# Kernel optimization log

Hardware: AMD Instinct MI355X
Metric: run time of the kernel (lower is better)

The kernel has to match this reference:

```python
import jax, jax.numpy as jnp
import numpy as np

N_NODES = 50000
N_EDGES = 500000
D_IN = 128
HID = 128
OUT = 2
N_REL = 4
BN_EPS = 1e-5


def setup_inputs() -> dict:
    key = jax.random.key(0)
    ks = jax.random.split(key, 14)
    s_in = 1.0 / np.sqrt(D_IN)
    s_h = 1.0 / np.sqrt(HID)
    return {
        "x": jax.random.normal(ks[0], (N_NODES, D_IN), jnp.float32),
        "edge_index": jax.random.randint(ks[1], (N_REL, 2, N_EDGES), 0, N_NODES, jnp.int32),
        "W1": jax.random.normal(ks[2], (N_REL, D_IN, HID), jnp.float32) * s_in,
        "b1": jax.random.normal(ks[3], (N_REL, HID), jnp.float32) * s_in,
        "W2": jax.random.normal(ks[4], (N_REL, HID, HID), jnp.float32) * s_h,
        "b2": jax.random.normal(ks[5], (N_REL, HID), jnp.float32) * s_h,
        "bn_gamma": jnp.ones((HID,), jnp.float32),
        "bn_beta": jnp.zeros((HID,), jnp.float32),
        "lin1_W": jax.random.normal(ks[6], (HID, HID), jnp.float32) * s_h,
        "lin1_b": jax.random.normal(ks[7], (HID,), jnp.float32) * s_h,
        "lin2_W": jax.random.normal(ks[8], (HID, OUT), jnp.float32) * s_h,
        "lin2_b": jax.random.normal(ks[9], (OUT,), jnp.float32) * s_h,
    }


def _gcn(x, ei, W, b):
    # GCNConv: D^-1/2 (A + I) D^-1/2 (X W) + b
    n = x.shape[0]
    h = x @ W                                    # [N, H]
    loops = jnp.arange(n, dtype=ei.dtype)
    src = jnp.concatenate([ei[0], loops])        # add self loops
    dst = jnp.concatenate([ei[1], loops])
    deg = jax.ops.segment_sum(jnp.ones(dst.shape, h.dtype), dst, num_segments=n)
    dinv = jnp.where(deg > 0, jax.lax.rsqrt(deg), 0.0)
    norm = dinv[src] * dinv[dst]                 # [E+N]
    msg = h[src] * norm[:, None]                 # gather + scale
    return jax.ops.segment_sum(msg, dst, num_segments=n) + b


def _hetero(x, edge_index, W, b):
    # HeteroConv with aggr='sum' over the 4 relation types (same src/dst node type)
    out = _gcn(x, edge_index[0], W[0], b[0])
    for r in range(1, N_REL):
        out = out + _gcn(x, edge_index[r], W[r], b[r])
    return out


def reference(x, edge_index, W1, b1, W2, b2, bn_gamma, bn_beta, lin1_W, lin1_b, lin2_W, lin2_b):
    h = jax.nn.relu(_hetero(x, edge_index, W1, b1))
    h = jax.nn.relu(_hetero(h, edge_index, W2, b2))
    # BatchNorm1d (batch statistics, biased variance)
    mean = h.mean(axis=0)
    var = h.var(axis=0)
    h = (h - mean) * jax.lax.rsqrt(var + BN_EPS) * bn_gamma + bn_beta
    h = jax.nn.relu(h @ lin1_W + lin1_b)
    # dropout is identity in eval
    return h @ lin2_W + lin2_b
```

## Files before the change

### kernel.cpp

```cpp
#include <hip/hip_runtime.h>
#include <math.h>

#define NN 50000
#define NE 500000
#define NREL 4
#define D 128
#define RSZ 512
#define NRANGE 98
#define NBK (NREL * NRANGE)
#define BCAP 6144
#define NCH 128
#define CH 3907
#define FCAP 96
#define CAST_BLKS 6250
static constexpr float BN_EPS = 1e-5f;

typedef __attribute__((ext_vector_type(8))) _Float16 half8;
typedef __attribute__((ext_vector_type(4))) float f32x4;

__device__ __forceinline__ unsigned short f2h_bits(float f) {
    _Float16 h = (_Float16)f;
    return __builtin_bit_cast(unsigned short, h);
}
__device__ __forceinline__ float hi2f(unsigned p) {
    return (float)__builtin_bit_cast(_Float16, (unsigned short)(p >> 16));
}

__global__ __launch_bounds__(256) void k_pre(const float* __restrict__ x,
                                             const float* __restrict__ W1, const float* __restrict__ W2,
                                             const float* __restrict__ l1W, const float* __restrict__ b1,
                                             const float* __restrict__ b2,
                                             unsigned short* __restrict__ xb,
                                             unsigned short* __restrict__ Wt1,
                                             unsigned short* __restrict__ Wt2,
                                             unsigned short* __restrict__ Wt3,
                                             float* __restrict__ bs1, float* __restrict__ bs2,
                                             float* __restrict__ bnsum) {
    int blk = blockIdx.x, tid = threadIdx.x;
    if (blk < CAST_BLKS) {
        int i = blk * 256 + tid;
        float4 v = *(const float4*)(x + (size_t)i * 4);
        unsigned short u[4] = {f2h_bits(v.x), f2h_bits(v.y), f2h_bits(v.z), f2h_bits(v.w)};
        *(ushort4*)(xb + (size_t)i * 4) = *(ushort4*)u;
    } else if (blk < CAST_BLKS + 256) {
        int i = (blk - CAST_BLKS) * 256 + tid;
        int kk = i & 511, n = i >> 9;
        Wt1[n * 512 + kk] = f2h_bits(W1[kk * 128 + n]);
        Wt2[n * 512 + kk] = f2h_bits(W2[kk * 128 + n]);
    } else if (blk < CAST_BLKS + 320) {
        int i = (blk - CAST_BLKS - 256) * 256 + tid;
        int kk = i & 127, n = i >> 7;
        Wt3[n * 128 + kk] = f2h_bits(l1W[kk * 128 + n]);
    } else {
        if (tid < 128) {
            bs1[tid] = b1[tid] + b1[128 + tid] + b1[256 + tid] + b1[384 + tid];
            bs2[tid] = b2[tid] + b2[128 + tid] + b2[256 + tid] + b2[384 + tid];
        }
        bnsum[tid] = 0.f;
    }
}

__global__ __launch_bounds__(256) void k_bin(const int* __restrict__ ei,
                                             int* __restrict__ frag,
                                             int* __restrict__ cntg) {
    int c = blockIdx.x, r = blockIdx.y;
    const int* srcp = ei + r * 2 * NE;
    const int* dstp = srcp + NE;
    __shared__ int bins[NRANGE * FCAP];
    __shared__ int cnt[NRANGE];
    int tid = threadIdx.x;
    for (int i = tid; i < NRANGE; i += 256) cnt[i] = 0;
    __syncthreads();
    int e0 = c * CH, e1 = min(e0 + CH, NE);
    for (int e = e0 + tid; e < e1; e += 256) {
        int d = dstp[e];
        int s = srcp[e];
        int q = d >> 9;
        int pos = atomicAdd(&cnt[q], 1);
        if (pos < FCAP) bins[q * FCAP + pos] = s | ((d & 511) << 16);
    }
    __syncthreads();
    int w = tid >> 6, lane = tid & 63;
    for (int q = w; q < NRANGE; q += 4) {
        int k = min(cnt[q], FCAP);
        int gbase = ((r * NRANGE + q) * NCH + c) * FCAP;
        for (int i = lane; i < k; i += 64) frag[gbase + i] = bins[q * FCAP + i];
    }
    for (int q = tid; q < NRANGE; q += 256) cntg[(r * NRANGE + q) * NCH + c] = min(cnt[q], FCAP);
}

__global__ __launch_bounds__(512) void k_sortb(const int* __restrict__ frag,
                                               const int* __restrict__ cntg,
                                               unsigned short* __restrict__ csr,
                                               int* __restrict__ rstart,
                                               int* __restrict__ rend,
                                               float* __restrict__ dinv) {
    int q = blockIdx.x, r = blockIdx.y;
    int blk = r * NRANGE + q;
    int n0 = q * RSZ;
    int nrows = min(RSZ, NN - n0);
    __shared__ int cnts[NCH], cbase[NCH];
    __shared__ int stage[BCAP];
    __shared__ unsigned short csr_s[BCAP];
    __shared__ int hist[RSZ], off[RSZ], cnt2[RSZ];
    int tid = threadIdx.x;
    hist[tid] = 0;
    cnt2[tid] = 0;
    if (tid < NCH) cnts[tid] = cntg[blk * NCH + tid];
    __syncthreads();
    if (tid < NCH) cbase[tid] = cnts[tid];
    __syncthreads();
    for (int d = 1; d < NCH; d <<= 1) {
        int t = 0;
        if (tid < NCH && tid >= d) t = cbase[tid - d];
        __syncthreads();
        if (tid < NCH) cbase[tid] += t;
        __syncthreads();
    }
    if (tid < NCH) cbase[tid] -= cnts[tid];
    __syncthreads();
    int tot = cbase[NCH - 1] + cnts[NCH - 1];
    {
        int g = tid >> 2, l = tid & 3;
        int k = cnts[g], cb = cbase[g];
        int gbase = (blk * NCH + g) * FCAP;
        for (int i = l; i < k; i += 4)
            if (cb + i < BCAP) stage[cb + i] = frag[gbase + i];
    }
    __syncthreads();
    if (tot > BCAP) tot = BCAP;
    for (int i = tid; i < tot; i += 512) atomicAdd(&hist[(stage[i] >> 16) & 511], 1);
    __syncthreads();
    int h = hist[tid];
    if (tid < nrows) dinv[r * NN + n0 + tid] = rsqrtf((float)(h + 1));
    off[tid] = h;
    __syncthreads();
    for (int d = 1; d < RSZ; d <<= 1) {
        int t = (tid >= d) ? off[tid - d] : 0;
        __syncthreads();
        off[tid] += t;
        __syncthreads();
    }
    int excl = off[tid] - h;
    __syncthreads();
    off[tid] = excl;
    int base = blk * BCAP;
    if (tid < nrows) {
        rstart[r * NN + n0 + tid] = base + excl;
        rend[r * NN + n0 + tid] = base + excl + h;
    }
    __syncthreads();
    for (int i = tid; i < tot; i += 512) {
        int v = stage[i];
        int dl = (v >> 16) & 511;
        int p = atomicAdd(&cnt2[dl], 1);
        csr_s[off[dl] + p] = (unsigned short)(v & 0xFFFF);
    }
    __syncthreads();
    for (int i = tid; i < tot; i += 512) csr[base + i] = csr_s[i];
}

__global__ __launch_bounds__(256) void k_wei(const unsigned short* __restrict__ csr,
                                             const float* __restrict__ dinv,
                                             unsigned* __restrict__ wpack) {
    int gi = blockIdx.x * 256 + threadIdx.x;
    int r = gi / (NRANGE * BCAP);
    int s = csr[gi];
    float w = dinv[r * NN + min(s, NN - 1)];
    wpack[gi] = (unsigned)s | ((unsigned)f2h_bits(w) << 16);
}

__global__ __launch_bounds__(256) void k_agg(const unsigned short* __restrict__ in,
                                             const unsigned* __restrict__ wpack,
                                             const int* __restrict__ rstart,
                                             const int* __restrict__ rend,
                                             const float* __restrict__ dinv,
                                             unsigned short* __restrict__ Acat) {
    int wave = threadIdx.x >> 6, lane = threadIdx.x & 63;
    int n = blockIdx.x * 4 + wave;
    if (n >= NN) return;
    int t = lane & 15;
    int base = lane & 48;
    int nb = (base >> 4) * NN + n;
    const half8* in8 = (const half8*)in;
    float wn = dinv[nb];
    int start = rstart[nb];
    int deg = rend[nb] - start;
    int dm = deg;
    dm = max(dm, __shfl_xor(dm, 16));
    dm = max(dm, __shfl_xor(dm, 32));
    half8 us = in8[(size_t)n * 16 + t];
    float a[8];
#pragma unroll
    for (int j = 0; j < 8; j++) a[j] = wn * (float)us[j];

    for (int w0 = 0; w0 < dm; w0 += 16) {
        int li = w0 + t;
        int gi = min(start + li, NBK * BCAP - 1);
        unsigned pv = wpack[gi];
        if (li >= deg) pv = 0u;
        unsigned p0 = __shfl(pv, base + 0), p1 = __shfl(pv, base + 1);
        unsigned p2 = __shfl(pv, base + 2), p3 = __shfl(pv, base + 3);
        unsigned p4 = __shfl(pv, base + 4), p5 = __shfl(pv, base + 5);
        unsigned p6 = __shfl(pv, base + 6), p7 = __shfl(pv, base + 7);
        {
            half8 r0 = in8[(p0 & 0xFFFFu) * 16 + t];
            half8 r1 = in8[(p1 & 0xFFFFu) * 16 + t];
            half8 r2 = in8[(p2 & 0xFFFFu) * 16 + t];
            half8 r3 = in8[(p3 & 0xFFFFu) * 16 + t];
            half8 r4 = in8[(p4 & 0xFFFFu) * 16 + t];
            half8 r5 = in8[(p5 & 0xFFFFu) * 16 + t];
            half8 r6 = in8[(p6 & 0xFFFFu) * 16 + t];
            half8 r7 = in8[(p7 & 0xFFFFu) * 16 + t];
            float w0f = hi2f(p0), w1f = hi2f(p1), w2f = hi2f(p2), w3f = hi2f(p3);
            float w4f = hi2f(p4), w5f = hi2f(p5), w6f = hi2f(p6), w7f = hi2f(p7);
#pragma unroll
            for (int j = 0; j < 8; j++) a[j] = fmaf((float)r0[j], w0f, a[j]);
#pragma unroll
            for (int j = 0; j < 8; j++) a[j] = fmaf((float)r1[j], w1f, a[j]);
#pragma unroll
            for (int j = 0; j < 8; j++) a[j] = fmaf((float)r2[j], w2f, a[j]);
#pragma unroll
            for (int j = 0; j < 8; j++) a[j] = fmaf((float)r3[j], w3f, a[j]);
#pragma unroll
            for (int j = 0; j < 8; j++) a[j] = fmaf((float)r4[j], w4f, a[j]);
#pragma unroll
            for (int j = 0; j < 8; j++) a[j] = fmaf((float)r5[j], w5f, a[j]);
#pragma unroll
            for (int j = 0; j < 8; j++) a[j] = fmaf((float)r6[j], w6f, a[j]);
#pragma unroll
            for (int j = 0; j < 8; j++) a[j] = fmaf((float)r7[j], w7f, a[j]);
        }
        if (w0 + 8 >= dm) continue;
        p0 = __shfl(pv, base + 8);  p1 = __shfl(pv, base + 9);
        p2 = __shfl(pv, base + 10); p3 = __shfl(pv, base + 11);
        p4 = __shfl(pv, base + 12); p5 = __shfl(pv, base + 13);
        p6 = __shfl(pv, base + 14); p7 = __shfl(pv, base + 15);
        {
            half8 r0 = in8[(p0 & 0xFFFFu) * 16 + t];
            half8 r1 = in8[(p1 & 0xFFFFu) * 16 + t];
            half8 r2 = in8[(p2 & 0xFFFFu) * 16 + t];
            half8 r3 = in8[(p3 & 0xFFFFu) * 16 + t];
            half8 r4 = in8[(p4 & 0xFFFFu) * 16 + t];
            half8 r5 = in8[(p5 & 0xFFFFu) * 16 + t];
            half8 r6 = in8[(p6 & 0xFFFFu) * 16 + t];
            half8 r7 = in8[(p7 & 0xFFFFu) * 16 + t];
            float w0f = hi2f(p0), w1f = hi2f(p1), w2f = hi2f(p2), w3f = hi2f(p3);
            float w4f = hi2f(p4), w5f = hi2f(p5), w6f = hi2f(p6), w7f = hi2f(p7);
#pragma unroll
            for (int j = 0; j < 8; j++) a[j] = fmaf((float)r0[j], w0f, a[j]);
#pragma unroll
            for (int j = 0; j < 8; j++) a[j] = fmaf((float)r1[j], w1f, a[j]);
#pragma unroll
            for (int j = 0; j < 8; j++) a[j] = fmaf((float)r2[j], w2f, a[j]);
#pragma unroll
            for (int j = 0; j < 8; j++) a[j] = fmaf((float)r3[j], w3f, a[j]);
#pragma unroll
            for (int j = 0; j < 8; j++) a[j] = fmaf((float)r4[j], w4f, a[j]);
#pragma unroll
            for (int j = 0; j < 8; j++) a[j] = fmaf((float)r5[j], w5f, a[j]);
#pragma unroll
            for (int j = 0; j < 8; j++) a[j] = fmaf((float)r6[j], w6f, a[j]);
#pragma unroll
            for (int j = 0; j < 8; j++) a[j] = fmaf((float)r7[j], w7f, a[j]);
        }
    }
    _Float16 ob[8];
#pragma unroll
    for (int j = 0; j < 8; j++) ob[j] = (_Float16)(wn * a[j]);
    *(half8*)(Acat + (size_t)n * 512 + (base << 3) + t * 8) = *(half8*)ob;
}

template <int K, bool STATS>
__global__ __launch_bounds__(256) void k_mm(const unsigned short* __restrict__ A,
                                            const unsigned short* __restrict__ Bt,
                                            const float* __restrict__ bias,
                                            unsigned short* __restrict__ C,
                                            float* __restrict__ bnsum) {
    int tid = threadIdx.x;
    int w = tid >> 6, lane = tid & 63;
    int ln = lane & 15, quad = lane >> 4;
    int mwave = blockIdx.x * 256 + w * 64;

    f32x4 acc[4][8];
#pragma unroll
    for (int a = 0; a < 4; a++)
#pragma unroll
        for (int b = 0; b < 8; b++) acc[a][b] = (f32x4){0.f, 0.f, 0.f, 0.f};

    size_t arow[4];
#pragma unroll
    for (int mf = 0; mf < 4; mf++) {
        int m = mwave + mf * 16 + ln;
        arow[mf] = (size_t)min(m, NN - 1) * K;
    }
    size_t brow[8];
#pragma unroll
    for (int nf = 0; nf < 8; nf++) brow[nf] = (size_t)(nf * 16 + ln) * K;

    for (int k0 = 0; k0 < K; k0 += 32) {
        int kof = k0 + quad * 8;
        half8 af[4], bf[8];
#pragma unroll
        for (int mf = 0; mf < 4; mf++) af[mf] = *(const half8*)(A + arow[mf] + kof);
#pragma unroll
        for (int nf = 0; nf < 8; nf++) bf[nf] = *(const half8*)(Bt + brow[nf] + kof);
#pragma unroll
        for (int mf = 0; mf < 4; mf++)
#pragma unroll
            for (int nf = 0; nf < 8; nf++)
                acc[mf][nf] = __builtin_amdgcn_mfma_f32_16x16x32_f16(af[mf], bf[nf], acc[mf][nf], 0, 0, 0);
    }

    float bs[8];
#pragma unroll
    for (int nf = 0; nf < 8; nf++) bs[nf] = bias[nf * 16 + ln];
    float sn[8], qn[8];
#pragma unroll
    for (int nf = 0; nf < 8; nf++) { sn[nf] = 0.f; qn[nf] = 0.f; }

#pragma unroll
    for (int mf = 0; mf < 4; mf++)
#pragma unroll
        for (int nf = 0; nf < 8; nf++)
#pragma unroll
            for (int rg = 0; rg < 4; rg++) {
                int m = mwave + mf * 16 + quad * 4 + rg;
                if (m < NN) {
                    float v = fmaxf(acc[mf][nf][rg] + bs[nf], 0.f);
                    if (STATS) { sn[nf] += v; qn[nf] += v * v; }
                    C[(size_t)m * 128 + nf * 16 + ln] = f2h_bits(v);
                }
            }

    if (STATS) {
#pragma unroll
        for (int nf = 0; nf < 8; nf++) {
            float s = sn[nf], q = qn[nf];
            s += __shfl_xor(s, 16); s += __shfl_xor(s, 32);
            q += __shfl_xor(q, 16); q += __shfl_xor(q, 32);
            if (quad == 0) {
                unsafeAtomicAdd(&bnsum[nf * 16 + ln], s);
                unsafeAtomicAdd(&bnsum[128 + nf * 16 + ln], q);
            }
        }
    }
}

__global__ __launch_bounds__(256) void k_final(const unsigned short* __restrict__ R2,
                                               const float* __restrict__ bnsum,
                                               const float* __restrict__ gamma,
                                               const float* __restrict__ beta,
                                               const unsigned short* __restrict__ Wt3,
                                               const float* __restrict__ l1b,
                                               const float* __restrict__ l2W,
                                               const float* __restrict__ l2b,
                                               float* __restrict__ out) {
    __shared__ float bnp_s[256];
    int tid = threadIdx.x;
    if (tid < 128) {
        float mean = bnsum[tid] / (float)NN;
        float var = bnsum[128 + tid] / (float)NN - mean * mean;
        float sc = gamma[tid] * rsqrtf(var + BN_EPS);
        bnp_s[tid] = sc;
        bnp_s[128 + tid] = beta[tid] - mean * sc;
    }
    __syncthreads();
    int w = tid >> 6, lane = tid & 63;
    int ln = lane & 15, quad = lane >> 4;
    int mwave = blockIdx.x * 256 + w * 64;

    f32x4 acc[4][8];
#pragma unroll
    for (int a = 0; a < 4; a++)
#pragma unroll
        for (int b = 0; b < 8; b++) acc[a][b] = (f32x4){0.f, 0.f, 0.f, 0.f};

    size_t arow[4];
#pragma unroll
    for (int mf = 0; mf < 4; mf++) {
        int m = mwave + mf * 16 + ln;
        arow[mf] = (size_t)min(m, NN - 1) * 128;
    }
    size_t brow[8];
#pragma unroll
    for (int nf = 0; nf < 8; nf++) brow[nf] = (size_t)(nf * 16 + ln) * 128;

    for (int k0 = 0; k0 < 128; k0 += 32) {
        int kof = k0 + quad * 8;
        float scv[8], shv[8];
#pragma unroll
        for (int j = 0; j < 8; j++) {
            scv[j] = bnp_s[kof + j];
            shv[j] = bnp_s[128 + kof + j];
        }
        half8 af[4], bf[8];
#pragma unroll
        for (int mf = 0; mf < 4; mf++) {
            half8 rv = *(const half8*)(R2 + arow[mf] + kof);
            _Float16 ab[8];
#pragma unroll
            for (int j = 0; j < 8; j++)
                ab[j] = (_Float16)(fmaf((float)rv[j], scv[j], shv[j]));
            af[mf] = *(half8*)ab;
        }
#pragma unroll
        for (int nf = 0; nf < 8; nf++) bf[nf] = *(const half8*)(Wt3 + brow[nf] + kof);
#pragma unroll
        for (int mf = 0; mf < 4; mf++)
#pragma unroll
            for (int nf = 0; nf < 8; nf++)
                acc[mf][nf] = __builtin_amdgcn_mfma_f32_16x16x32_f16(af[mf], bf[nf], acc[mf][nf], 0, 0, 0);
    }

    float b1v[8], w0[8], w1[8];
#pragma unroll
    for (int nf = 0; nf < 8; nf++) {
        int n = nf * 16 + ln;
        b1v[nf] = l1b[n];
        w0[nf] = l2W[n * 2];
        w1[nf] = l2W[n * 2 + 1];
    }
    float ob0 = l2b[0], ob1 = l2b[1];
#pragma unroll
    for (int mf = 0; mf < 4; mf++)
#pragma unroll
        for (int rg = 0; rg < 4; rg++) {
            float p0 = 0.f, p1 = 0.f;
#pragma unroll
            for (int nf = 0; nf < 8; nf++) {
                float y = fmaxf(acc[mf][nf][rg] + b1v[nf], 0.f);
                p0 += y * w0[nf];
                p1 += y * w1[nf];
            }
            p0 += __shfl_xor(p0, 1); p0 += __shfl_xor(p0, 2);
            p0 += __shfl_xor(p0, 4); p0 += __shfl_xor(p0, 8);
            p1 += __shfl_xor(p1, 1); p1 += __shfl_xor(p1, 2);
            p1 += __shfl_xor(p1, 4); p1 += __shfl_xor(p1, 8);
            int m = mwave + mf * 16 + quad * 4 + rg;
            if (ln == 0 && m < NN) {
                out[(size_t)m * 2 + 0] = p0 + ob0;
                out[(size_t)m * 2 + 1] = p1 + ob1;
            }
        }
}

extern "C" void kernel_launch(void* const* d_in, const int* in_sizes, int n_in,
                              void* d_out, int out_size, void* d_ws, size_t ws_size,
                              hipStream_t stream) {
    const float* x = (const float*)d_in[0];
    const int* ei = (const int*)d_in[1];
    const float* W1 = (const float*)d_in[2];
    const float* b1 = (const float*)d_in[3];
    const float* W2 = (const float*)d_in[4];
    const float* b2 = (const float*)d_in[5];
    const float* gamma = (const float*)d_in[6];
    const float* beta = (const float*)d_in[7];
    const float* l1W = (const float*)d_in[8];
    const float* l1b = (const float*)d_in[9];
    const float* l2W = (const float*)d_in[10];
    const float* l2b = (const float*)d_in[11];
    float* out = (float*)d_out;

    char* ws = (char*)d_ws;
    size_t off = 0;
    auto alloc = [&](size_t bytes) {
        void* p = ws + off;
        off += (bytes + 255) & ~(size_t)255;
        return p;
    };
    float* dinv = (float*)alloc((size_t)NREL * NN * sizeof(float));
    int* rstart = (int*)alloc((size_t)NREL * NN * sizeof(int));
    int* rend = (int*)alloc((size_t)NREL * NN * sizeof(int));
    unsigned short* csr = (unsigned short*)alloc((size_t)NBK * BCAP * 2);
    unsigned short* xb = (unsigned short*)alloc((size_t)NN * D * 2);
    unsigned short* Acat = (unsigned short*)alloc((size_t)NN * 512 * 2);
    unsigned short* h1b = (unsigned short*)alloc((size_t)NN * D * 2);
    unsigned short* R2b = (unsigned short*)alloc((size_t)NN * D * 2);
    unsigned short* Wt1 = (unsigned short*)alloc(128 * 512 * 2);
    unsigned short* Wt2 = (unsigned short*)alloc(128 * 512 * 2);
    unsigned short* Wt3 = (unsigned short*)alloc(128 * 128 * 2);
    float* bs1 = (float*)alloc(128 * sizeof(float));
    float* bs2 = (float*)alloc(128 * sizeof(float));
    float* bnsum = (float*)alloc(256 * sizeof(float));

    int* frag = (int*)Acat;
    int* cntg = frag + (size_t)NREL * NRANGE * NCH * FCAP;
    unsigned* wpack = (unsigned*)R2b;

    k_pre<<<CAST_BLKS + 321, 256, 0, stream>>>(x, W1, W2, l1W, b1, b2, xb, Wt1, Wt2, Wt3,
                                               bs1, bs2, bnsum);
    dim3 bgrid(NCH, NREL);
    k_bin<<<bgrid, 256, 0, stream>>>(ei, frag, cntg);
    dim3 sgrid(NRANGE, NREL);
    k_sortb<<<sgrid, 512, 0, stream>>>(frag, cntg, csr, rstart, rend, dinv);
    k_wei<<<(NBK * BCAP) / 256, 256, 0, stream>>>(csr, dinv, wpack);

    int agrid = (NN + 3) / 4;
    k_agg<<<agrid, 256, 0, stream>>>(xb, wpack, rstart, rend, dinv, Acat);
    k_mm<512, false><<<(NN + 255) / 256, 256, 0, stream>>>(Acat, Wt1, bs1, h1b, nullptr);
    k_agg<<<agrid, 256, 0, stream>>>(h1b, wpack, rstart, rend, dinv, Acat);
    k_mm<512, true><<<(NN + 255) / 256, 256, 0, stream>>>(Acat, Wt2, bs2, R2b, bnsum);
    k_final<<<(NN + 255) / 256, 256, 0, stream>>>(R2b, bnsum, gamma, beta, Wt3, l1b, l2W, l2b, out);
}
```

Baseline: 367.8 us.

## Fuse neighbor aggregation with MFMA matmul via shared-memory tile

```diff
diff --git a/kernel.cpp b/kernel.cpp
--- a/kernel.cpp
+++ b/kernel.cpp
@@ -13,6 +13,9 @@
 #define CH 3907
 #define FCAP 96
 #define CAST_BLKS 6250
+#define TN 32
+#define NPW 8
+#define NTILE ((NN + TN - 1) / TN)
 static constexpr float BN_EPS = 1e-5f;
 
 typedef __attribute__((ext_vector_type(8))) _Float16 half8;
@@ -170,178 +173,191 @@
     wpack[gi] = (unsigned)s | ((unsigned)f2h_bits(w) << 16);
 }
 
-__global__ __launch_bounds__(256) void k_agg(const unsigned short* __restrict__ in,
-                                             const unsigned* __restrict__ wpack,
-                                             const int* __restrict__ rstart,
-                                             const int* __restrict__ rend,
-                                             const float* __restrict__ dinv,
-                                             unsigned short* __restrict__ Acat) {
-    int wave = threadIdx.x >> 6, lane = threadIdx.x & 63;
-    int n = blockIdx.x * 4 + wave;
-    if (n >= NN) return;
+template <bool STATS>
+__global__ __launch_bounds__(256) void k_fused(const unsigned short* __restrict__ in,
+                                               const unsigned* __restrict__ wpack,
+                                               const int* __restrict__ rstart,
+                                               const int* __restrict__ rend,
+                                               const float* __restrict__ dinv,
+                                               const unsigned short* __restrict__ Bt,
+                                               const float* __restrict__ bias,
+                                               unsigned short* __restrict__ C,
+                                               float* __restrict__ bnsum) {
+    __shared__ unsigned short A_s[TN * 512];
+    int tid = threadIdx.x;
+    int wave = tid >> 6, lane = tid & 63;
     int t = lane & 15;
     int base = lane & 48;
-    int nb = (base >> 4) * NN + n;
+    int q = base >> 4;
+    int tile = blockIdx.x;
     const half8* in8 = (const half8*)in;
-    float wn = dinv[nb];
-    int start = rstart[nb];
-    int deg = rend[nb] - start;
-    int dm = deg;
-    dm = max(dm, __shfl_xor(dm, 16));
-    dm = max(dm, __shfl_xor(dm, 32));
-    half8 us = in8[(size_t)n * 16 + t];
-    float a[8];
-#pragma unroll
-    for (int j = 0; j < 8; j++) a[j] = wn * (float)us[j];
-
-    for (int w0 = 0; w0 < dm; w0 += 16) {
-        int li = w0 + t;
-        int gi = min(start + li, NBK * BCAP - 1);
-        unsigned pv = wpack[gi];
-        if (li >= deg) pv = 0u;
-        unsigned p0 = __shfl(pv, base + 0), p1 = __shfl(pv, base + 1);
-        unsigned p2 = __shfl(pv, base + 2), p3 = __shfl(pv, base + 3);
-        unsigned p4 = __shfl(pv, base + 4), p5 = __shfl(pv, base + 5);
-        unsigned p6 = __shfl(pv, base + 6), p7 = __shfl(pv, base + 7);
-        {
-            half8 r0 = in8[(p0 & 0xFFFFu) * 16 + t];
-            half8 r1 = in8[(p1 & 0xFFFFu) * 16 + t];
-            half8 r2 = in8[(p2 & 0xFFFFu) * 16 + t];
-            half8 r3 = in8[(p3 & 0xFFFFu) * 16 + t];
-            half8 r4 = in8[(p4 & 0xFFFFu) * 16 + t];
-            half8 r5 = in8[(p5 & 0xFFFFu) * 16 + t];
-            half8 r6 = in8[(p6 & 0xFFFFu) * 16 + t];
-            half8 r7 = in8[(p7 & 0xFFFFu) * 16 + t];
-            float w0f = hi2f(p0), w1f = hi2f(p1), w2f = hi2f(p2), w3f = hi2f(p3);
-            float w4f = hi2f(p4), w5f = hi2f(p5), w6f = hi2f(p6), w7f = hi2f(p7);
-#pragma unroll
-            for (int j = 0; j < 8; j++) a[j] = fmaf((float)r0[j], w0f, a[j]);
-#pragma unroll
-            for (int j = 0; j < 8; j++) a[j] = fmaf((float)r1[j], w1f, a[j]);
-#pragma unroll
-            for (int j = 0; j < 8; j++) a[j] = fmaf((float)r2[j], w2f, a[j]);
-#pragma unroll
-            for (int j = 0; j < 8; j++) a[j] = fmaf((float)r3[j], w3f, a[j]);
-#pragma unroll
-            for (int j = 0; j < 8; j++) a[j] = fmaf((float)r4[j], w4f, a[j]);
-#pragma unroll
-            for (int j = 0; j < 8; j++) a[j] = fmaf((float)r5[j], w5f, a[j]);
-#pragma unroll
-            for (int j = 0; j < 8; j++) a[j] = fmaf((float)r6[j], w6f, a[j]);
-#pragma unroll
-            for (int j = 0; j < 8; j++) a[j] = fmaf((float)r7[j], w7f, a[j]);
-        }
-        if (w0 + 8 >= dm) continue;
-        p0 = __shfl(pv, base + 8);  p1 = __shfl(pv, base + 9);
-        p2 = __shfl(pv, base + 10); p3 = __shfl(pv, base + 11);
-        p4 = __shfl(pv, base + 12); p5 = __shfl(pv, base + 13);
-        p6 = __shfl(pv, base + 14); p7 = __shfl(pv, base + 15);
-        {
-            half8 r0 = in8[(p0 & 0xFFFFu) * 16 + t];
-            half8 r1 = in8[(p1 & 0xFFFFu) * 16 + t];
-            half8 r2 = in8[(p2 & 0xFFFFu) * 16 + t];
-            half8 r3 = in8[(p3 & 0xFFFFu) * 16 + t];
-            half8 r4 = in8[(p4 & 0xFFFFu) * 16 + t];
-            half8 r5 = in8[(p5 & 0xFFFFu) * 16 + t];
-            half8 r6 = in8[(p6 & 0xFFFFu) * 16 + t];
-            half8 r7 = in8[(p7 & 0xFFFFu) * 16 + t];
-            float w0f = hi2f(p0), w1f = hi2f(p1), w2f = hi2f(p2), w3f = hi2f(p3);
-            float w4f = hi2f(p4), w5f = hi2f(p5), w6f = hi2f(p6), w7f = hi2f(p7);
-#pragma unroll
-            for (int j = 0; j < 8; j++) a[j] = fmaf((float)r0[j], w0f, a[j]);
-#pragma unroll
-            for (int j = 0; j < 8; j++) a[j] = fmaf((float)r1[j], w1f, a[j]);
-#pragma unroll
-            for (int j = 0; j < 8; j++) a[j] = fmaf((float)r2[j], w2f, a[j]);
-#pragma unroll
-            for (int j = 0; j < 8; j++) a[j] = fmaf((float)r3[j], w3f, a[j]);
-#pragma unroll
-            for (int j = 0; j < 8; j++) a[j] = fmaf((float)r4[j], w4f, a[j]);
-#pragma unroll
-            for (int j = 0; j < 8; j++) a[j] = fmaf((float)r5[j], w5f, a[j]);
-#pragma unroll
-            for (int j = 0; j < 8; j++) a[j] = fmaf((float)r6[j], w6f, a[j]);
-#pragma unroll
-            for (int j = 0; j < 8; j++) a[j] = fmaf((float)r7[j], w7f, a[j]);
-        }
-    }
-    _Float16 ob[8];
-#pragma unroll
-    for (int j = 0; j < 8; j++) ob[j] = (_Float16)(wn * a[j]);
-    *(half8*)(Acat + (size_t)n * 512 + (base << 3) + t * 8) = *(half8*)ob;
-}
-
-template <int K, bool STATS>
-__global__ __launch_bounds__(256) void k_mm(const unsigned short* __restrict__ A,
-                                            const unsigned short* __restrict__ Bt,
-                                            const float* __restrict__ bias,
-                                            unsigned short* __restrict__ C,
-                                            float* __restrict__ bnsum) {
-    int tid = threadIdx.x;
-    int w = tid >> 6, lane = tid & 63;
+    int nbq = q * NN;
+
+    int row0 = wave * NPW;
+    {
+        int n0 = tile * TN + row0;
+        int nc0 = min(n0, NN - 1);
+        int sP = rstart[nbq + nc0];
+        int eP = rend[nbq + nc0];
+        float wP = dinv[nbq + nc0];
+        half8 uP = in8[(size_t)nc0 * 16 + t];
+        for (int i = 0; i < NPW; ++i) {
+            int row = row0 + i;
+            int n = tile * TN + row;
+            bool valid = (n < NN);
+            int start = sP;
+            int deg = valid ? (eP - sP) : 0;
+            float wn = valid ? wP : 0.f;
+            half8 us = uP;
+            if (i + 1 < NPW) {
+                int nn = min(n + 1, NN - 1);
+                sP = rstart[nbq + nn];
+                eP = rend[nbq + nn];
+                wP = dinv[nbq + nn];
+                uP = in8[(size_t)nn * 16 + t];
+            }
+            int dm = deg;
+            dm = max(dm, __shfl_xor(dm, 16));
+            dm = max(dm, __shfl_xor(dm, 32));
+            float a[8];
+#pragma unroll
+            for (int j = 0; j < 8; j++) a[j] = wn * (float)us[j];
+
+            for (int w0 = 0; w0 < dm; w0 += 16) {
+                int li = w0 + t;
+                int gi = min(start + li, NBK * BCAP - 1);
+                unsigned pv = wpack[gi];
+                if (li >= deg) pv = 0u;
+                unsigned p0 = __shfl(pv, base + 0), p1 = __shfl(pv, base + 1);
+                unsigned p2 = __shfl(pv, base + 2), p3 = __shfl(pv, base + 3);
+                unsigned p4 = __shfl(pv, base + 4), p5 = __shfl(pv, base + 5);
+                unsigned p6 = __shfl(pv, base + 6), p7 = __shfl(pv, base + 7);
+                {
+                    half8 r0 = in8[(p0 & 0xFFFFu) * 16 + t];
+                    half8 r1 = in8[(p1 & 0xFFFFu) * 16 + t];
+                    half8 r2 = in8[(p2 & 0xFFFFu) * 16 + t];
+                    half8 r3 = in8[(p3 & 0xFFFFu) * 16 + t];
+                    half8 r4 = in8[(p4 & 0xFFFFu) * 16 + t];
+                    half8 r5 = in8[(p5 & 0xFFFFu) * 16 + t];
+                    half8 r6 = in8[(p6 & 0xFFFFu) * 16 + t];
+                    half8 r7 = in8[(p7 & 0xFFFFu) * 16 + t];
+                    float w0f = hi2f(p0), w1f = hi2f(p1), w2f = hi2f(p2), w3f = hi2f(p3);
+                    float w4f = hi2f(p4), w5f = hi2f(p5), w6f = hi2f(p6), w7f = hi2f(p7);
+#pragma unroll
+                    for (int j = 0; j < 8; j++) a[j] = fmaf((float)r0[j], w0f, a[j]);
+#pragma unroll
+                    for (int j = 0; j < 8; j++) a[j] = fmaf((float)r1[j], w1f, a[j]);
+#pragma unroll
+                    for (int j = 0; j < 8; j++) a[j] = fmaf((float)r2[j], w2f, a[j]);
+#pragma unroll
+                    for (int j = 0; j < 8; j++) a[j] = fmaf((float)r3[j], w3f, a[j]);
+#pragma unroll
+                    for (int j = 0; j < 8; j++) a[j] = fmaf((float)r4[j], w4f, a[j]);
+#pragma unroll
+                    for (int j = 0; j < 8; j++) a[j] = fmaf((float)r5[j], w5f, a[j]);
+#pragma unroll
+                    for (int j = 0; j < 8; j++) a[j] = fmaf((float)r6[j], w6f, a[j]);
+#pragma unroll
+                    for (int j = 0; j < 8; j++) a[j] = fmaf((float)r7[j], w7f, a[j]);
+                }
+                if (w0 + 8 >= dm) continue;
+                p0 = __shfl(pv, base + 8);  p1 = __shfl(pv, base + 9);
+                p2 = __shfl(pv, base + 10); p3 = __shfl(pv, base + 11);
+                p4 = __shfl(pv, base + 12); p5 = __shfl(pv, base + 13);
+                p6 = __shfl(pv, base + 14); p7 = __shfl(pv, base + 15);
+                {
+                    half8 r0 = in8[(p0 & 0xFFFFu) * 16 + t];
+                    half8 r1 = in8[(p1 & 0xFFFFu) * 16 + t];
+                    half8 r2 = in8[(p2 & 0xFFFFu) * 16 + t];
+                    half8 r3 = in8[(p3 & 0xFFFFu) * 16 + t];
+                    half8 r4 = in8[(p4 & 0xFFFFu) * 16 + t];
+                    half8 r5 = in8[(p5 & 0xFFFFu) * 16 + t];
+                    half8 r6 = in8[(p6 & 0xFFFFu) * 16 + t];
+                    half8 r7 = in8[(p7 & 0xFFFFu) * 16 + t];
+                    float w0f = hi2f(p0), w1f = hi2f(p1), w2f = hi2f(p2), w3f = hi2f(p3);
+                    float w4f = hi2f(p4), w5f = hi2f(p5), w6f = hi2f(p6), w7f = hi2f(p7);
+#pragma unroll
+                    for (int j = 0; j < 8; j++) a[j] = fmaf((float)r0[j], w0f, a[j]);
+#pragma unroll
+                    for (int j = 0; j < 8; j++) a[j] = fmaf((float)r1[j], w1f, a[j]);
+#pragma unroll
+                    for (int j = 0; j < 8; j++) a[j] = fmaf((float)r2[j], w2f, a[j]);
+#pragma unroll
+                    for (int j = 0; j < 8; j++) a[j] = fmaf((float)r3[j], w3f, a[j]);
+#pragma unroll
+                    for (int j = 0; j < 8; j++) a[j] = fmaf((float)r4[j], w4f, a[j]);
+#pragma unroll
+                    for (int j = 0; j < 8; j++) a[j] = fmaf((float)r5[j], w5f, a[j]);
+#pragma unroll
+                    for (int j = 0; j < 8; j++) a[j] = fmaf((float)r6[j], w6f, a[j]);
+#pragma unroll
+                    for (int j = 0; j < 8; j++) a[j] = fmaf((float)r7[j], w7f, a[j]);
+                }
+            }
+            _Float16 ob[8];
+#pragma unroll
+            for (int j = 0; j < 8; j++) ob[j] = (_Float16)(wn * a[j]);
+            int offb = row * 1024 + ((lane * 16) ^ ((row & 7) << 4));
+            *(half8*)((char*)A_s + offb) = *(half8*)ob;
+        }
+    }
+    __syncthreads();
+
     int ln = lane & 15, quad = lane >> 4;
-    int mwave = blockIdx.x * 256 + w * 64;
-
-    f32x4 acc[4][8];
-#pragma unroll
-    for (int a = 0; a < 4; a++)
-#pragma unroll
-        for (int b = 0; b < 8; b++) acc[a][b] = (f32x4){0.f, 0.f, 0.f, 0.f};
-
-    size_t arow[4];
-#pragma unroll
-    for (int mf = 0; mf < 4; mf++) {
-        int m = mwave + mf * 16 + ln;
-        arow[mf] = (size_t)min(m, NN - 1) * K;
-    }
-    size_t brow[8];
-#pragma unroll
-    for (int nf = 0; nf < 8; nf++) brow[nf] = (size_t)(nf * 16 + ln) * K;
-
-    for (int k0 = 0; k0 < K; k0 += 32) {
-        int kof = k0 + quad * 8;
-        half8 af[4], bf[8];
-#pragma unroll
-        for (int mf = 0; mf < 4; mf++) af[mf] = *(const half8*)(A + arow[mf] + kof);
-#pragma unroll
-        for (int nf = 0; nf < 8; nf++) bf[nf] = *(const half8*)(Bt + brow[nf] + kof);
-#pragma unroll
-        for (int mf = 0; mf < 4; mf++)
-#pragma unroll
-            for (int nf = 0; nf < 8; nf++)
+    f32x4 acc[2][2];
+#pragma unroll
+    for (int a = 0; a < 2; a++)
+#pragma unroll
+        for (int b = 0; b < 2; b++) acc[a][b] = (f32x4){0.f, 0.f, 0.f, 0.f};
+    size_t brow[2];
+#pragma unroll
+    for (int nf = 0; nf < 2; nf++) brow[nf] = (size_t)(wave * 32 + nf * 16 + ln) * 512;
+
+    for (int k0 = 0; k0 < 512; k0 += 32) {
+        int kofb = k0 * 2 + quad * 16;
+        half8 af[2], bf[2];
+#pragma unroll
+        for (int mf = 0; mf < 2; mf++) {
+            int rr = mf * 16 + ln;
+            int offb = rr * 1024 + (kofb ^ ((rr & 7) << 4));
+            af[mf] = *(const half8*)((const char*)A_s + offb);
+        }
+#pragma unroll
+        for (int nf = 0; nf < 2; nf++) bf[nf] = *(const half8*)(Bt + brow[nf] + (kofb >> 1));
+#pragma unroll
+        for (int mf = 0; mf < 2; mf++)
+#pragma unroll
+            for (int nf = 0; nf < 2; nf++)
                 acc[mf][nf] = __builtin_amdgcn_mfma_f32_16x16x32_f16(af[mf], bf[nf], acc[mf][nf], 0, 0, 0);
     }
 
-    float bs[8];
-#pragma unroll
-    for (int nf = 0; nf < 8; nf++) bs[nf] = bias[nf * 16 + ln];
-    float sn[8], qn[8];
-#pragma unroll
-    for (int nf = 0; nf < 8; nf++) { sn[nf] = 0.f; qn[nf] = 0.f; }
-
-#pragma unroll
-    for (int mf = 0; mf < 4; mf++)
-#pragma unroll
-        for (int nf = 0; nf < 8; nf++)
+    float bs[2];
+#pragma unroll
+    for (int nf = 0; nf < 2; nf++) bs[nf] = bias[wave * 32 + nf * 16 + ln];
+    float sn[2] = {0.f, 0.f}, qn[2] = {0.f, 0.f};
+#pragma unroll
+    for (int mf = 0; mf < 2; mf++)
+#pragma unroll
+        for (int nf = 0; nf < 2; nf++)
 #pragma unroll
             for (int rg = 0; rg < 4; rg++) {
-                int m = mwave + mf * 16 + quad * 4 + rg;
+                int m = tile * TN + mf * 16 + quad * 4 + rg;
                 if (m < NN) {
                     float v = fmaxf(acc[mf][nf][rg] + bs[nf], 0.f);
                     if (STATS) { sn[nf] += v; qn[nf] += v * v; }
-                    C[(size_t)m * 128 + nf * 16 + ln] = f2h_bits(v);
+                    C[(size_t)m * 128 + wave * 32 + nf * 16 + ln] = f2h_bits(v);
                 }
             }
-
     if (STATS) {
 #pragma unroll
-        for (int nf = 0; nf < 8; nf++) {
-            float s = sn[nf], q = qn[nf];
+        for (int nf = 0; nf < 2; nf++) {
+            float s = sn[nf], qq = qn[nf];
             s += __shfl_xor(s, 16); s += __shfl_xor(s, 32);
-            q += __shfl_xor(q, 16); q += __shfl_xor(q, 32);
+            qq += __shfl_xor(qq, 16); qq += __shfl_xor(qq, 32);
             if (quad == 0) {
-                unsafeAtomicAdd(&bnsum[nf * 16 + ln], s);
-                unsafeAtomicAdd(&bnsum[128 + nf * 16 + ln], q);
+                int col = wave * 32 + nf * 16 + ln;
+                unsafeAtomicAdd(&bnsum[col], s);
+                unsafeAtomicAdd(&bnsum[128 + col], qq);
             }
         }
     }
@@ -473,8 +489,8 @@
     int* rstart = (int*)alloc((size_t)NREL * NN * sizeof(int));
     int* rend = (int*)alloc((size_t)NREL * NN * sizeof(int));
     unsigned short* csr = (unsigned short*)alloc((size_t)NBK * BCAP * 2);
+    unsigned* wpack = (unsigned*)alloc((size_t)NBK * BCAP * 4);
     unsigned short* xb = (unsigned short*)alloc((size_t)NN * D * 2);
-    unsigned short* Acat = (unsigned short*)alloc((size_t)NN * 512 * 2);
     unsigned short* h1b = (unsigned short*)alloc((size_t)NN * D * 2);
     unsigned short* R2b = (unsigned short*)alloc((size_t)NN * D * 2);
     unsigned short* Wt1 = (unsigned short*)alloc(128 * 512 * 2);
@@ -483,10 +499,8 @@
     float* bs1 = (float*)alloc(128 * sizeof(float));
     float* bs2 = (float*)alloc(128 * sizeof(float));
     float* bnsum = (float*)alloc(256 * sizeof(float));
-
-    int* frag = (int*)Acat;
-    int* cntg = frag + (size_t)NREL * NRANGE * NCH * FCAP;
-    unsigned* wpack = (unsigned*)R2b;
+    int* frag = (int*)alloc((size_t)NREL * NRANGE * NCH * FCAP * 4);
+    int* cntg = (int*)alloc((size_t)NREL * NRANGE * NCH * 4);
 
     k_pre<<<CAST_BLKS + 321, 256, 0, stream>>>(x, W1, W2, l1W, b1, b2, xb, Wt1, Wt2, Wt3,
                                                bs1, bs2, bnsum);
@@ -496,10 +510,7 @@
     k_sortb<<<sgrid, 512, 0, stream>>>(frag, cntg, csr, rstart, rend, dinv);
     k_wei<<<(NBK * BCAP) / 256, 256, 0, stream>>>(csr, dinv, wpack);
 
-    int agrid = (NN + 3) / 4;
-    k_agg<<<agrid, 256, 0, stream>>>(xb, wpack, rstart, rend, dinv, Acat);
-    k_mm<512, false><<<(NN + 255) / 256, 256, 0, stream>>>(Acat, Wt1, bs1, h1b, nullptr);
-    k_agg<<<agrid, 256, 0, stream>>>(h1b, wpack, rstart, rend, dinv, Acat);
-    k_mm<512, true><<<(NN + 255) / 256, 256, 0, stream>>>(Acat, Wt2, bs2, R2b, bnsum);
+    k_fused<false><<<NTILE, 256, 0, stream>>>(xb, wpack, rstart, rend, dinv, Wt1, bs1, h1b, nullptr);
+    k_fused<true><<<NTILE, 256, 0, stream>>>(h1b, wpack, rstart, rend, dinv, Wt2, bs2, R2b, bnsum);
     k_final<<<(NN + 255) / 256, 256, 0, stream>>>(R2b, bnsum, gamma, beta, Wt3, l1b, l2W, l2b, out);
 }
```

Result: faster. 358.9 us (-2.4%).
